# Optimization experiments

Measured on AMD Instinct MI355X. Metric: run time of the kernel, lower is better.

Reference implementation:

```python
import jax, jax.numpy as jnp
import numpy as np

GENE_DIM = 3000
DRUG_DIM = 2048
K = 6          # num_neurons_per_GO
KF = 24        # num_neurons_per_final_GO
T0, T1 = 1500, 400
OUT0, OUT1, OUT2 = T0 * K, T1 * K, KF
B = 256
NF = 64        # num_neurons_final
ND = [128, 64, 32]
EPS = 1e-5


def _edges():
    rng = np.random.default_rng(0)
    # level 0: each of T0 terms gets 30 genes, expanded to K neurons per term
    t = np.repeat(np.arange(T0), 30)
    g = rng.integers(0, GENE_DIM, T0 * 30)
    rows0 = (t[:, None] * K + np.arange(K)).ravel()
    cols0 = np.repeat(g, K)
    # level 1: each of T1 terms has 5 children among T0 terms, kron with ones(K,K)
    o = np.repeat(np.arange(T1), 5)
    c = rng.integers(0, T0, T1 * 5)
    P = len(o)
    rows1 = np.repeat(o, K * K) * K + np.tile(np.repeat(np.arange(K), K), P)
    cols1 = np.repeat(c, K * K) * K + np.tile(np.tile(np.arange(K), K), P)
    # level 2: single root with all T1 children, KF output neurons x K input neurons
    rows2 = np.tile(np.repeat(np.arange(KF), K), T1)
    cols2 = np.repeat(np.arange(T1), KF * K) * K + np.tile(np.arange(K), T1 * KF)
    return [(jnp.asarray(r, jnp.int32), jnp.asarray(cc, jnp.int32))
            for r, cc in ((rows0, cols0), (rows1, cols1), (rows2, cols2))]


def setup_inputs() -> dict:
    key = jax.random.key(0)
    ks = iter(jax.random.split(key, 64))
    (rows0, cols0), (rows1, cols1), (rows2, cols2) = _edges()
    nrm = lambda shape, s=0.1: s * jax.random.normal(next(ks), shape, jnp.float32)
    inp = {
        'x': jax.random.normal(next(ks), (B, GENE_DIM + DRUG_DIM), jnp.float32),
        'rows0': rows0, 'cols0': cols0, 'w0': nrm((rows0.shape[0],)), 'b0': nrm((OUT0,), 0.01),
        'rows1': rows1, 'cols1': cols1, 'w1': nrm((rows1.shape[0],)), 'b1': nrm((OUT1,), 0.01),
        'rows2': rows2, 'cols2': cols2, 'w2': nrm((rows2.shape[0],)), 'b2': nrm((OUT2,), 0.01),
        'gg': 1.0 + nrm((GENE_DIM,)), 'eg': nrm((GENE_DIM,), 0.01),
        'g1': 1.0 + nrm((OUT0,)), 'e1': nrm((OUT0,), 0.01),
        'g2': 1.0 + nrm((OUT1,)), 'e2': nrm((OUT1,), 0.01),
    }
    fan = DRUG_DIM
    for i, n in enumerate(ND, 1):
        inp[f'Wd{i}'] = nrm((n, fan), 1.0 / np.sqrt(fan))
        inp[f'bd{i}'] = nrm((n,), 0.01)
        inp[f'gd{i}'] = 1.0 + nrm((fan,))
        inp[f'ed{i}'] = nrm((fan,), 0.01)
        fan = n
    fin = KF + ND[-1]
    inp.update({
        'gf': 1.0 + nrm((fin,)), 'ef': nrm((fin,), 0.01),
        'Wf': nrm((NF, fin), 1.0 / np.sqrt(fin)), 'bf': nrm((NF,), 0.01),
        'ga': 1.0 + nrm((NF,)), 'ea': nrm((NF,), 0.01),
        'Wa': nrm((1, NF), 1.0 / np.sqrt(NF)), 'ba': nrm((1,), 0.01),
        'Wo': nrm((1, 1), 1.0), 'bo': nrm((1,), 0.01),
    })
    return inp


def _bn(x, g, e):
    # BatchNorm1d, training-mode batch statistics (biased var), dropout p=0
    mu = jnp.mean(x, 0)
    var = jnp.var(x, 0)
    return g * (x - mu) * jax.lax.rsqrt(var + EPS) + e


def _splin(x, rows, cols, w, b, n_out):
    # SparseLinear: y[b, rows[e]] += w[e] * x[b, cols[e]]
    data = (x[:, cols] * w).T                       # [E, B]
    return jax.ops.segment_sum(data, rows, num_segments=n_out).T + b


def reference(x, rows0, cols0, w0, b0, rows1, cols1, w1, b1, rows2, cols2, w2, b2,
              gg, eg, g1, e1, g2, e2,
              Wd1, bd1, gd1, ed1, Wd2, bd2, gd2, ed2, Wd3, bd3, gd3, ed3,
              gf, ef, Wf, bf, ga, ea, Wa, ba, Wo, bo):
    gene = x[:, :GENE_DIM]
    drug = x[:, GENE_DIM:GENE_DIM + DRUG_DIM]
    h = _bn(gene, gg, eg)
    h = jnp.tanh(_splin(h, rows0, cols0, w0, b0, OUT0))
    h = _bn(h, g1, e1)
    h = jnp.tanh(_splin(h, rows1, cols1, w1, b1, OUT1))
    h = _bn(h, g2, e2)
    h = jnp.tanh(_splin(h, rows2, cols2, w2, b2, OUT2))
    d = drug
    for (W, bb, g, e) in ((Wd1, bd1, gd1, ed1), (Wd2, bd2, gd2, ed2), (Wd3, bd3, gd3, ed3)):
        d = jnp.tanh(_bn(d, g, e) @ W.T + bb)
    o = _bn(jnp.concatenate([h, d], 1), gf, ef)
    o = jnp.tanh(o @ Wf.T + bf)
    o = _bn(o, ga, ea)
    o = jnp.tanh(o @ Wa.T + ba)
    return o @ Wo.T + bo
```

## Files before the change

kernel.cpp:

```cpp
#include <hip/hip_runtime.h>
#include <math.h>

#define NB 256
#define XW 5048
#define GENE 3000
#define DRUGW 2048
#define EPSF 1e-5f

template<int NR>
__device__ __forceinline__ void bn_fold_write(float (&v)[NR], int b,
        const float* __restrict__ g, const float* __restrict__ e,
        float* __restrict__ out_t) {
    __shared__ float sred[NR][4][2];
    __shared__ float s_ac[2][NR];
    int lane = b & 63, wv = b >> 6;
    float s1[NR], s2[NR];
    #pragma unroll
    for (int k = 0; k < NR; k++) { s1[k] = v[k]; s2[k] = v[k] * v[k]; }
    #pragma unroll
    for (int off = 32; off >= 1; off >>= 1) {
        #pragma unroll
        for (int k = 0; k < NR; k++) {
            s1[k] += __shfl_xor(s1[k], off);
            s2[k] += __shfl_xor(s2[k], off);
        }
    }
    if (lane == 0) {
        #pragma unroll
        for (int k = 0; k < NR; k++) { sred[k][wv][0] = s1[k]; sred[k][wv][1] = s2[k]; }
    }
    __syncthreads();
    if (b < NR) {
        float t1 = sred[b][0][0] + sred[b][1][0] + sred[b][2][0] + sred[b][3][0];
        float t2 = sred[b][0][1] + sred[b][1][1] + sred[b][2][1] + sred[b][3][1];
        float mu  = t1 * (1.0f / 256.0f);
        float var = t2 * (1.0f / 256.0f) - mu * mu;
        float rs  = rsqrtf(var + EPSF);
        float aa  = g[b] * rs;
        s_ac[0][b] = aa;
        s_ac[1][b] = e[b] - aa * mu;
    }
    __syncthreads();
    #pragma unroll
    for (int k = 0; k < NR; k++)
        out_t[k * NB + b] = s_ac[0][k] * v[k] + s_ac[1][k];
}

__global__ void k_in_bn(const float* __restrict__ x,
                        const float* __restrict__ gg, const float* __restrict__ eg,
                        const float* __restrict__ gd, const float* __restrict__ ed,
                        float* __restrict__ gene_n, float* __restrict__ drug_n) {
    __shared__ float tile[32 * 257];
    __shared__ float red1[8][33], red2[8][33];
    __shared__ float s_a[32], s_c[32];
    int t = threadIdx.x;
    int tx = t & 31, ty = t >> 5;
    int c0 = blockIdx.x * 32;
    int c = c0 + tx;
    bool valid = c < XW;
    float s1 = 0.f, s2 = 0.f;
    #pragma unroll 4
    for (int i = 0; i < 32; i++) {
        int r = ty * 32 + i;
        float v = valid ? x[(size_t)r * XW + c] : 0.f;
        tile[tx * 257 + r] = v;
        s1 += v; s2 += v * v;
    }
    red1[ty][tx] = s1; red2[ty][tx] = s2;
    __syncthreads();
    if (t < 32) {
        float t1 = 0.f, t2 = 0.f;
        #pragma unroll
        for (int k = 0; k < 8; k++) { t1 += red1[k][t]; t2 += red2[k][t]; }
        float mu  = t1 * (1.0f / 256.0f);
        float var = t2 * (1.0f / 256.0f) - mu * mu;
        float rs  = rsqrtf(var + EPSF);
        int col = c0 + t;
        float gv = 0.f, ev = 0.f;
        if (col < GENE)      { gv = gg[col];        ev = eg[col]; }
        else if (col < XW)   { gv = gd[col - GENE]; ev = ed[col - GENE]; }
        float aa = gv * rs;
        s_a[t] = aa; s_c[t] = ev - aa * mu;
    }
    __syncthreads();
    for (int cc = 0; cc < 32; cc++) {
        int col = c0 + cc;
        if (col >= XW) break;
        float w = s_a[cc] * tile[cc * 257 + t] + s_c[cc];
        if (col < GENE) gene_n[(size_t)col * NB + t] = w;
        else            drug_n[(size_t)(col - GENE) * NB + t] = w;
    }
}

__global__ void k_splin0(const float* __restrict__ gene_n,
                         const int* __restrict__ cols0, const float* __restrict__ w0,
                         const float* __restrict__ b0,
                         const float* __restrict__ g1, const float* __restrict__ e1,
                         float* __restrict__ h1n) {
    int t = blockIdx.x, b = threadIdx.x;
    float acc[6] = {0.f, 0.f, 0.f, 0.f, 0.f, 0.f};
    int base = t * 180;
    for (int i = 0; i < 30; i++) {
        int ei = base + i * 6;
        int cc = cols0[ei];
        float v = gene_n[(size_t)cc * NB + b];
        #pragma unroll
        for (int k = 0; k < 6; k++) acc[k] += v * w0[ei + k];
    }
    float v6[6];
    #pragma unroll
    for (int k = 0; k < 6; k++) v6[k] = tanhf(acc[k] + b0[t * 6 + k]);
    bn_fold_write<6>(v6, b, g1 + t * 6, e1 + t * 6, h1n + (size_t)t * 6 * NB);
}

__global__ void k_splin1(const float* __restrict__ h1n,
                         const int* __restrict__ cols1, const float* __restrict__ w1,
                         const float* __restrict__ b1,
                         const float* __restrict__ g2, const float* __restrict__ e2,
                         float* __restrict__ h2n) {
    int o = blockIdx.x, b = threadIdx.x;
    float acc[6] = {0.f, 0.f, 0.f, 0.f, 0.f, 0.f};
    for (int pi = 0; pi < 5; pi++) {
        int qb = (o * 5 + pi) * 36;
        #pragma unroll
        for (int j = 0; j < 6; j++) {
            int cc = cols1[qb + j];
            float v = h1n[(size_t)cc * NB + b];
            #pragma unroll
            for (int i = 0; i < 6; i++) acc[i] += v * w1[qb + i * 6 + j];
        }
    }
    float v6[6];
    #pragma unroll
    for (int i = 0; i < 6; i++) v6[i] = tanhf(acc[i] + b1[o * 6 + i]);
    bn_fold_write<6>(v6, b, g2 + o * 6, e2 + o * 6, h2n + (size_t)o * 6 * NB);
}

__global__ void k_splin2_part(const float* __restrict__ h2n,
                              const float* __restrict__ w2,
                              float* __restrict__ part2) {
    int kf = blockIdx.x >> 4, ch = blockIdx.x & 15, b = threadIdx.x;
    float acc = 0.f;
    int t0 = ch * 25;
    for (int t = t0; t < t0 + 25; t++) {
        const float* wrow = w2 + t * 144 + kf * 6;
        #pragma unroll
        for (int j = 0; j < 6; j++)
            acc += h2n[(size_t)(t * 6 + j) * NB + b] * wrow[j];
    }
    part2[(size_t)blockIdx.x * NB + b] = acc;
}

__global__ void k_splin2_fin(const float* __restrict__ part2,
                             const float* __restrict__ b2,
                             const float* __restrict__ gf, const float* __restrict__ ef,
                             float* __restrict__ fbn) {
    int kf = blockIdx.x, b = threadIdx.x;
    float acc = b2[kf];
    #pragma unroll
    for (int ch = 0; ch < 16; ch++) acc += part2[(size_t)(kf * 16 + ch) * NB + b];
    float v[1] = { tanhf(acc) };
    bn_fold_write<1>(v, b, gf + kf, ef + kf, fbn + (size_t)kf * NB);
}

__global__ void k_dense1_part(const float* __restrict__ drug_n,
                              const float* __restrict__ Wd1,
                              float* __restrict__ part1) {
    int jg = blockIdx.x >> 3, ch = blockIdx.x & 7, b = threadIdx.x;
    int j0 = jg * 4, c0 = ch * 256;
    float acc[4] = {0.f, 0.f, 0.f, 0.f};
    for (int c = c0; c < c0 + 256; c++) {
        float v = drug_n[(size_t)c * NB + b];
        #pragma unroll
        for (int jj = 0; jj < 4; jj++) acc[jj] += v * Wd1[(size_t)(j0 + jj) * DRUGW + c];
    }
    #pragma unroll
    for (int jj = 0; jj < 4; jj++)
        part1[(size_t)((j0 + jj) * 8 + ch) * NB + b] = acc[jj];
}

__global__ void k_dense1_fin(const float* __restrict__ part1,
                             const float* __restrict__ bd1,
                             const float* __restrict__ gd2, const float* __restrict__ ed2,
                             float* __restrict__ d1n) {
    int j = blockIdx.x, b = threadIdx.x;
    float acc = bd1[j];
    #pragma unroll
    for (int ch = 0; ch < 8; ch++) acc += part1[(size_t)(j * 8 + ch) * NB + b];
    float v[1] = { tanhf(acc) };
    bn_fold_write<1>(v, b, gd2 + j, ed2 + j, d1n + (size_t)j * NB);
}

template<int JPB>
__global__ void k_dense_n(const float* __restrict__ in_n,
                          const float* __restrict__ W, const float* __restrict__ bias,
                          int ncols,
                          const float* __restrict__ g, const float* __restrict__ e,
                          float* __restrict__ out_n) {
    int j0 = blockIdx.x * JPB, b = threadIdx.x;
    float acc[JPB];
    #pragma unroll
    for (int jj = 0; jj < JPB; jj++) acc[jj] = 0.f;
    for (int c = 0; c < ncols; c++) {
        float v = in_n[(size_t)c * NB + b];
        #pragma unroll
        for (int jj = 0; jj < JPB; jj++) acc[jj] += v * W[(size_t)(j0 + jj) * ncols + c];
    }
    float v[JPB];
    #pragma unroll
    for (int jj = 0; jj < JPB; jj++) v[jj] = tanhf(acc[jj] + bias[j0 + jj]);
    bn_fold_write<JPB>(v, b, g + j0, e + j0, out_n + (size_t)j0 * NB);
}

__global__ void k_final(const float* __restrict__ o1n,
                        const float* __restrict__ Wa, const float* __restrict__ ba,
                        const float* __restrict__ Wo, const float* __restrict__ bo,
                        float* __restrict__ out) {
    int b = threadIdx.x;
    float acc = ba[0];
    #pragma unroll
    for (int j = 0; j < 64; j++) acc += o1n[(size_t)j * NB + b] * Wa[j];
    out[b] = tanhf(acc) * Wo[0] + bo[0];
}

extern "C" void kernel_launch(void* const* d_in, const int* in_sizes, int n_in,
                              void* d_out, int out_size, void* d_ws, size_t ws_size,
                              hipStream_t stream) {
    const float* x    = (const float*)d_in[0];
    const int*   cols0 = (const int*)d_in[2];
    const float* w0   = (const float*)d_in[3];
    const float* b0   = (const float*)d_in[4];
    const int*   cols1 = (const int*)d_in[6];
    const float* w1   = (const float*)d_in[7];
    const float* b1   = (const float*)d_in[8];
    const float* w2   = (const float*)d_in[11];
    const float* b2   = (const float*)d_in[12];
    const float* gg   = (const float*)d_in[13];
    const float* eg   = (const float*)d_in[14];
    const float* g1   = (const float*)d_in[15];
    const float* e1   = (const float*)d_in[16];
    const float* g2   = (const float*)d_in[17];
    const float* e2   = (const float*)d_in[18];
    const float* Wd1  = (const float*)d_in[19];
    const float* bd1  = (const float*)d_in[20];
    const float* gd1  = (const float*)d_in[21];
    const float* ed1  = (const float*)d_in[22];
    const float* Wd2  = (const float*)d_in[23];
    const float* bd2  = (const float*)d_in[24];
    const float* gd2  = (const float*)d_in[25];
    const float* ed2  = (const float*)d_in[26];
    const float* Wd3  = (const float*)d_in[27];
    const float* bd3  = (const float*)d_in[28];
    const float* gd3  = (const float*)d_in[29];
    const float* ed3  = (const float*)d_in[30];
    const float* gf   = (const float*)d_in[31];
    const float* ef   = (const float*)d_in[32];
    const float* Wf   = (const float*)d_in[33];
    const float* bf   = (const float*)d_in[34];
    const float* ga   = (const float*)d_in[35];
    const float* ea   = (const float*)d_in[36];
    const float* Wa   = (const float*)d_in[37];
    const float* ba   = (const float*)d_in[38];
    const float* Wo   = (const float*)d_in[39];
    const float* bo   = (const float*)d_in[40];
    float* out = (float*)d_out;

    float* W = (float*)d_ws;
    float* gene_n = W;
    float* drug_n = gene_n + 3000 * NB;
    float* h1n    = drug_n + 2048 * NB;
    float* h2n    = h1n    + 9000 * NB;
    float* fbn    = h2n    + 2400 * NB;
    float* d1n    = fbn    + 56 * NB;
    float* d2n    = d1n    + 128 * NB;
    float* o1n    = d2n    + 64 * NB;
    float* part2  = o1n    + 64 * NB;
    float* part1  = part2  + 24 * 16 * NB;

    k_in_bn<<<(XW + 31) / 32, 256, 0, stream>>>(x, gg, eg, gd1, ed1, gene_n, drug_n);

    k_splin0<<<1500, 256, 0, stream>>>(gene_n, cols0, w0, b0, g1, e1, h1n);
    k_splin1<<<400, 256, 0, stream>>>(h1n, cols1, w1, b1, g2, e2, h2n);
    k_splin2_part<<<24 * 16, 256, 0, stream>>>(h2n, w2, part2);
    k_splin2_fin<<<24, 256, 0, stream>>>(part2, b2, gf, ef, fbn);

    k_dense1_part<<<32 * 8, 256, 0, stream>>>(drug_n, Wd1, part1);
    k_dense1_fin<<<128, 256, 0, stream>>>(part1, bd1, gd2, ed2, d1n);
    k_dense_n<8><<<8, 256, 0, stream>>>(d1n, Wd2, bd2, 128, gd3, ed3, d2n);
    k_dense_n<8><<<4, 256, 0, stream>>>(d2n, Wd3, bd3, 64, gf + 24, ef + 24, fbn + 24 * NB);

    k_dense_n<8><<<8, 256, 0, stream>>>(fbn, Wf, bf, 56, ga, ea, o1n);
    k_final<<<1, 256, 0, stream>>>(o1n, Wa, ba, Wo, bo, out);
}
```

Baseline: 148.9 us.

## Fuse all stages into one persistent kernel with atomic grid barriers

Replaces the eleven separate kernel launches with a single persistent kernel of 256 blocks. Stages are separated by a software grid barrier built on an atomic counter, and independent work such as the gene and drug branches is packed into the same phase. Intermediate activations h1 and h2 are stored batch-interleaved so later stages can use float2 loads, and splin2 now computes all 24 outputs per chunk. This removes launch gaps and per-kernel tails, at the cost of spin-wait barriers, lower parallelism in the small stages, and a memset launch to reset the counter.

```diff
diff --git a/kernel.cpp b/kernel.cpp
--- a/kernel.cpp
+++ b/kernel.cpp
@@ -6,11 +6,49 @@
 #define GENE 3000
 #define DRUGW 2048
 #define EPSF 1e-5f
-
-template<int NR>
-__device__ __forceinline__ void bn_fold_write(float (&v)[NR], int b,
+#define NBLK 256
+
+struct Params {
+    const float* x;
+    const int* cols0; const float* w0; const float* b0;
+    const int* cols1; const float* w1; const float* b1;
+    const float* w2;  const float* b2;
+    const float* gg;  const float* eg;
+    const float* g1;  const float* e1;
+    const float* g2;  const float* e2;
+    const float* Wd1; const float* bd1;
+    const float* gd1; const float* ed1;
+    const float* Wd2; const float* bd2;
+    const float* gd2; const float* ed2;
+    const float* Wd3; const float* bd3;
+    const float* gd3; const float* ed3;
+    const float* gf;  const float* ef;
+    const float* Wf;  const float* bf;
+    const float* ga;  const float* ea;
+    const float* Wa;  const float* ba;
+    const float* Wo;  const float* bo;
+    float* out;
+    float* gene_n; float* drug_n; float* h1i; float* h2i;
+    float* fbn; float* d1n; float* d2n; float* o1n; float* part2; float* part1;
+    unsigned int* bar;
+};
+
+__device__ __forceinline__ void gbar(unsigned int* bar, unsigned int target) {
+    __syncthreads();
+    if (threadIdx.x == 0) {
+        __threadfence();
+        __hip_atomic_fetch_add(bar, 1u, __ATOMIC_RELEASE, __HIP_MEMORY_SCOPE_AGENT);
+        while (__hip_atomic_load(bar, __ATOMIC_ACQUIRE, __HIP_MEMORY_SCOPE_AGENT) < target)
+            __builtin_amdgcn_s_sleep(2);
+        __threadfence();
+    }
+    __syncthreads();
+}
+
+template<int NR, bool ILEAVE>
+__device__ __forceinline__ void bn_fold(float (&v)[NR], int b,
         const float* __restrict__ g, const float* __restrict__ e,
-        float* __restrict__ out_t) {
+        float* __restrict__ out) {
     __shared__ float sred[NR][4][2];
     __shared__ float s_ac[2][NR];
     int lane = b & 63, wv = b >> 6;
@@ -42,43 +80,40 @@
     }
     __syncthreads();
     #pragma unroll
-    for (int k = 0; k < NR; k++)
-        out_t[k * NB + b] = s_ac[0][k] * v[k] + s_ac[1][k];
-}
-
-__global__ void k_in_bn(const float* __restrict__ x,
-                        const float* __restrict__ gg, const float* __restrict__ eg,
-                        const float* __restrict__ gd, const float* __restrict__ ed,
-                        float* __restrict__ gene_n, float* __restrict__ drug_n) {
-    __shared__ float tile[32 * 257];
-    __shared__ float red1[8][33], red2[8][33];
-    __shared__ float s_a[32], s_c[32];
-    int t = threadIdx.x;
+    for (int k = 0; k < NR; k++) {
+        float w = s_ac[0][k] * v[k] + s_ac[1][k];
+        if (ILEAVE) out[b * NR + k] = w;
+        else        out[k * NB + b] = w;
+    }
+}
+
+__device__ __forceinline__ void inbn_task(const Params& p, int task, int t,
+        float* tile, float* red1, float* red2, float* s_a, float* s_c) {
     int tx = t & 31, ty = t >> 5;
-    int c0 = blockIdx.x * 32;
+    int c0 = task * 32;
     int c = c0 + tx;
     bool valid = c < XW;
     float s1 = 0.f, s2 = 0.f;
     #pragma unroll 4
     for (int i = 0; i < 32; i++) {
         int r = ty * 32 + i;
-        float v = valid ? x[(size_t)r * XW + c] : 0.f;
+        float v = valid ? p.x[(size_t)r * XW + c] : 0.f;
         tile[tx * 257 + r] = v;
         s1 += v; s2 += v * v;
     }
-    red1[ty][tx] = s1; red2[ty][tx] = s2;
+    red1[ty * 33 + tx] = s1; red2[ty * 33 + tx] = s2;
     __syncthreads();
     if (t < 32) {
         float t1 = 0.f, t2 = 0.f;
         #pragma unroll
-        for (int k = 0; k < 8; k++) { t1 += red1[k][t]; t2 += red2[k][t]; }
+        for (int k = 0; k < 8; k++) { t1 += red1[k * 33 + t]; t2 += red2[k * 33 + t]; }
         float mu  = t1 * (1.0f / 256.0f);
         float var = t2 * (1.0f / 256.0f) - mu * mu;
         float rs  = rsqrtf(var + EPSF);
         int col = c0 + t;
         float gv = 0.f, ev = 0.f;
-        if (col < GENE)      { gv = gg[col];        ev = eg[col]; }
-        else if (col < XW)   { gv = gd[col - GENE]; ev = ed[col - GENE]; }
+        if (col < GENE)      { gv = p.gg[col];         ev = p.eg[col]; }
+        else if (col < XW)   { gv = p.gd1[col - GENE]; ev = p.ed1[col - GENE]; }
         float aa = gv * rs;
         s_a[t] = aa; s_c[t] = ev - aa * mu;
     }
@@ -87,208 +122,223 @@
         int col = c0 + cc;
         if (col >= XW) break;
         float w = s_a[cc] * tile[cc * 257 + t] + s_c[cc];
-        if (col < GENE) gene_n[(size_t)col * NB + t] = w;
-        else            drug_n[(size_t)(col - GENE) * NB + t] = w;
-    }
-}
-
-__global__ void k_splin0(const float* __restrict__ gene_n,
-                         const int* __restrict__ cols0, const float* __restrict__ w0,
-                         const float* __restrict__ b0,
-                         const float* __restrict__ g1, const float* __restrict__ e1,
-                         float* __restrict__ h1n) {
-    int t = blockIdx.x, b = threadIdx.x;
+        if (col < GENE) p.gene_n[(size_t)col * NB + t] = w;
+        else            p.drug_n[(size_t)(col - GENE) * NB + t] = w;
+    }
+    __syncthreads();
+}
+
+__device__ __forceinline__ void splin0_task(const Params& p, int t, int b) {
     float acc[6] = {0.f, 0.f, 0.f, 0.f, 0.f, 0.f};
     int base = t * 180;
     for (int i = 0; i < 30; i++) {
         int ei = base + i * 6;
-        int cc = cols0[ei];
-        float v = gene_n[(size_t)cc * NB + b];
-        #pragma unroll
-        for (int k = 0; k < 6; k++) acc[k] += v * w0[ei + k];
+        int cc = p.cols0[ei];
+        float v = p.gene_n[(size_t)cc * NB + b];
+        #pragma unroll
+        for (int k = 0; k < 6; k++) acc[k] += v * p.w0[ei + k];
     }
     float v6[6];
     #pragma unroll
-    for (int k = 0; k < 6; k++) v6[k] = tanhf(acc[k] + b0[t * 6 + k]);
-    bn_fold_write<6>(v6, b, g1 + t * 6, e1 + t * 6, h1n + (size_t)t * 6 * NB);
-}
-
-__global__ void k_splin1(const float* __restrict__ h1n,
-                         const int* __restrict__ cols1, const float* __restrict__ w1,
-                         const float* __restrict__ b1,
-                         const float* __restrict__ g2, const float* __restrict__ e2,
-                         float* __restrict__ h2n) {
-    int o = blockIdx.x, b = threadIdx.x;
+    for (int k = 0; k < 6; k++) v6[k] = tanhf(acc[k] + p.b0[t * 6 + k]);
+    bn_fold<6, true>(v6, b, p.g1 + t * 6, p.e1 + t * 6, p.h1i + (size_t)t * 6 * NB);
+}
+
+__device__ __forceinline__ void splin1_task(const Params& p, int o, int b) {
     float acc[6] = {0.f, 0.f, 0.f, 0.f, 0.f, 0.f};
     for (int pi = 0; pi < 5; pi++) {
         int qb = (o * 5 + pi) * 36;
-        #pragma unroll
-        for (int j = 0; j < 6; j++) {
-            int cc = cols1[qb + j];
-            float v = h1n[(size_t)cc * NB + b];
+        int cbase = p.cols1[qb];
+        const float* hv = p.h1i + (size_t)cbase * NB + b * 6;
+        const float2* hv2 = (const float2*)hv;
+        float2 a0 = hv2[0], a1 = hv2[1], a2 = hv2[2];
+        float v[6] = {a0.x, a0.y, a1.x, a1.y, a2.x, a2.y};
+        #pragma unroll
+        for (int j = 0; j < 6; j++)
             #pragma unroll
-            for (int i = 0; i < 6; i++) acc[i] += v * w1[qb + i * 6 + j];
-        }
+            for (int i = 0; i < 6; i++) acc[i] += v[j] * p.w1[qb + i * 6 + j];
     }
     float v6[6];
     #pragma unroll
-    for (int i = 0; i < 6; i++) v6[i] = tanhf(acc[i] + b1[o * 6 + i]);
-    bn_fold_write<6>(v6, b, g2 + o * 6, e2 + o * 6, h2n + (size_t)o * 6 * NB);
-}
-
-__global__ void k_splin2_part(const float* __restrict__ h2n,
-                              const float* __restrict__ w2,
-                              float* __restrict__ part2) {
-    int kf = blockIdx.x >> 4, ch = blockIdx.x & 15, b = threadIdx.x;
-    float acc = 0.f;
+    for (int i = 0; i < 6; i++) v6[i] = tanhf(acc[i] + p.b1[o * 6 + i]);
+    bn_fold<6, true>(v6, b, p.g2 + o * 6, p.e2 + o * 6, p.h2i + (size_t)o * 6 * NB);
+}
+
+__device__ __forceinline__ void splin2_part_task(const Params& p, int ch, int b) {
+    float acc[24];
+    #pragma unroll
+    for (int kf = 0; kf < 24; kf++) acc[kf] = 0.f;
     int t0 = ch * 25;
     for (int t = t0; t < t0 + 25; t++) {
-        const float* wrow = w2 + t * 144 + kf * 6;
-        #pragma unroll
-        for (int j = 0; j < 6; j++)
-            acc += h2n[(size_t)(t * 6 + j) * NB + b] * wrow[j];
-    }
-    part2[(size_t)blockIdx.x * NB + b] = acc;
-}
-
-__global__ void k_splin2_fin(const float* __restrict__ part2,
-                             const float* __restrict__ b2,
-                             const float* __restrict__ gf, const float* __restrict__ ef,
-                             float* __restrict__ fbn) {
-    int kf = blockIdx.x, b = threadIdx.x;
-    float acc = b2[kf];
-    #pragma unroll
-    for (int ch = 0; ch < 16; ch++) acc += part2[(size_t)(kf * 16 + ch) * NB + b];
+        const float* hv = p.h2i + (size_t)t * 6 * NB + b * 6;
+        const float2* hv2 = (const float2*)hv;
+        float2 a0 = hv2[0], a1 = hv2[1], a2 = hv2[2];
+        float v[6] = {a0.x, a0.y, a1.x, a1.y, a2.x, a2.y};
+        const float* wr = p.w2 + t * 144;
+        #pragma unroll
+        for (int kf = 0; kf < 24; kf++)
+            #pragma unroll
+            for (int j = 0; j < 6; j++) acc[kf] += v[j] * wr[kf * 6 + j];
+    }
+    #pragma unroll
+    for (int kf = 0; kf < 24; kf++)
+        p.part2[(size_t)(ch * 24 + kf) * NB + b] = acc[kf];
+}
+
+__device__ __forceinline__ void splin2_fin_task(const Params& p, int kf, int b) {
+    float acc = p.b2[kf];
+    #pragma unroll
+    for (int ch = 0; ch < 16; ch++) acc += p.part2[(size_t)(ch * 24 + kf) * NB + b];
     float v[1] = { tanhf(acc) };
-    bn_fold_write<1>(v, b, gf + kf, ef + kf, fbn + (size_t)kf * NB);
-}
-
-__global__ void k_dense1_part(const float* __restrict__ drug_n,
-                              const float* __restrict__ Wd1,
-                              float* __restrict__ part1) {
-    int jg = blockIdx.x >> 3, ch = blockIdx.x & 7, b = threadIdx.x;
+    bn_fold<1, false>(v, b, p.gf + kf, p.ef + kf, p.fbn + (size_t)kf * NB);
+}
+
+__device__ __forceinline__ void dense1_part_task(const Params& p, int sub, int b) {
+    int jg = sub >> 3, ch = sub & 7;
     int j0 = jg * 4, c0 = ch * 256;
     float acc[4] = {0.f, 0.f, 0.f, 0.f};
     for (int c = c0; c < c0 + 256; c++) {
-        float v = drug_n[(size_t)c * NB + b];
-        #pragma unroll
-        for (int jj = 0; jj < 4; jj++) acc[jj] += v * Wd1[(size_t)(j0 + jj) * DRUGW + c];
+        float v = p.drug_n[(size_t)c * NB + b];
+        #pragma unroll
+        for (int jj = 0; jj < 4; jj++) acc[jj] += v * p.Wd1[(size_t)(j0 + jj) * DRUGW + c];
     }
     #pragma unroll
     for (int jj = 0; jj < 4; jj++)
-        part1[(size_t)((j0 + jj) * 8 + ch) * NB + b] = acc[jj];
-}
-
-__global__ void k_dense1_fin(const float* __restrict__ part1,
-                             const float* __restrict__ bd1,
-                             const float* __restrict__ gd2, const float* __restrict__ ed2,
-                             float* __restrict__ d1n) {
-    int j = blockIdx.x, b = threadIdx.x;
-    float acc = bd1[j];
-    #pragma unroll
-    for (int ch = 0; ch < 8; ch++) acc += part1[(size_t)(j * 8 + ch) * NB + b];
+        p.part1[(size_t)((j0 + jj) * 8 + ch) * NB + b] = acc[jj];
+}
+
+__device__ __forceinline__ void dense1_fin_task(const Params& p, int j, int b) {
+    float acc = p.bd1[j];
+    #pragma unroll
+    for (int ch = 0; ch < 8; ch++) acc += p.part1[(size_t)(j * 8 + ch) * NB + b];
     float v[1] = { tanhf(acc) };
-    bn_fold_write<1>(v, b, gd2 + j, ed2 + j, d1n + (size_t)j * NB);
-}
-
-template<int JPB>
-__global__ void k_dense_n(const float* __restrict__ in_n,
-                          const float* __restrict__ W, const float* __restrict__ bias,
-                          int ncols,
-                          const float* __restrict__ g, const float* __restrict__ e,
-                          float* __restrict__ out_n) {
-    int j0 = blockIdx.x * JPB, b = threadIdx.x;
-    float acc[JPB];
-    #pragma unroll
-    for (int jj = 0; jj < JPB; jj++) acc[jj] = 0.f;
+    bn_fold<1, false>(v, b, p.gd2 + j, p.ed2 + j, p.d1n + (size_t)j * NB);
+}
+
+__device__ __forceinline__ void dense8_task(const float* __restrict__ in_n,
+        const float* __restrict__ W, const float* __restrict__ bias, int ncols,
+        const float* __restrict__ g, const float* __restrict__ e,
+        float* __restrict__ out_n, int j0, int b) {
+    float acc[8] = {0.f,0.f,0.f,0.f,0.f,0.f,0.f,0.f};
     for (int c = 0; c < ncols; c++) {
         float v = in_n[(size_t)c * NB + b];
         #pragma unroll
-        for (int jj = 0; jj < JPB; jj++) acc[jj] += v * W[(size_t)(j0 + jj) * ncols + c];
-    }
-    float v[JPB];
-    #pragma unroll
-    for (int jj = 0; jj < JPB; jj++) v[jj] = tanhf(acc[jj] + bias[j0 + jj]);
-    bn_fold_write<JPB>(v, b, g + j0, e + j0, out_n + (size_t)j0 * NB);
-}
-
-__global__ void k_final(const float* __restrict__ o1n,
-                        const float* __restrict__ Wa, const float* __restrict__ ba,
-                        const float* __restrict__ Wo, const float* __restrict__ bo,
-                        float* __restrict__ out) {
-    int b = threadIdx.x;
-    float acc = ba[0];
-    #pragma unroll
-    for (int j = 0; j < 64; j++) acc += o1n[(size_t)j * NB + b] * Wa[j];
-    out[b] = tanhf(acc) * Wo[0] + bo[0];
+        for (int jj = 0; jj < 8; jj++) acc[jj] += v * W[(size_t)(j0 + jj) * ncols + c];
+    }
+    float v[8];
+    #pragma unroll
+    for (int jj = 0; jj < 8; jj++) v[jj] = tanhf(acc[jj] + bias[j0 + jj]);
+    bn_fold<8, false>(v, b, g + j0, e + j0, out_n + (size_t)j0 * NB);
+}
+
+__device__ __forceinline__ void final_task(const Params& p, int b) {
+    float acc = p.ba[0];
+    #pragma unroll
+    for (int j = 0; j < 64; j++) acc += p.o1n[(size_t)j * NB + b] * p.Wa[j];
+    p.out[b] = tanhf(acc) * p.Wo[0] + p.bo[0];
+}
+
+__global__ __launch_bounds__(256) void k_mega(Params p) {
+    __shared__ float tile[32 * 257];
+    __shared__ float red1[8 * 33];
+    __shared__ float red2[8 * 33];
+    __shared__ float s_a[32], s_c[32];
+    const int b = threadIdx.x;
+
+    for (int task = blockIdx.x; task < 158; task += gridDim.x)
+        inbn_task(p, task, b, tile, red1, red2, s_a, s_c);
+    gbar(p.bar, 1 * NBLK);
+
+    for (int task = blockIdx.x; task < 1756; task += gridDim.x) {
+        if (task < 1500) splin0_task(p, task, b);
+        else             dense1_part_task(p, task - 1500, b);
+    }
+    gbar(p.bar, 2 * NBLK);
+
+    for (int task = blockIdx.x; task < 528; task += gridDim.x) {
+        if (task < 400) splin1_task(p, task, b);
+        else            dense1_fin_task(p, task - 400, b);
+    }
+    gbar(p.bar, 3 * NBLK);
+
+    for (int task = blockIdx.x; task < 24; task += gridDim.x) {
+        if (task < 16) splin2_part_task(p, task, b);
+        else dense8_task(p.d1n, p.Wd2, p.bd2, 128, p.gd3, p.ed3, p.d2n, (task - 16) * 8, b);
+    }
+    gbar(p.bar, 4 * NBLK);
+
+    for (int task = blockIdx.x; task < 28; task += gridDim.x) {
+        if (task < 24) splin2_fin_task(p, task, b);
+        else dense8_task(p.d2n, p.Wd3, p.bd3, 64, p.gf + 24, p.ef + 24,
+                         p.fbn + 24 * NB, (task - 24) * 8, b);
+    }
+    gbar(p.bar, 5 * NBLK);
+
+    for (int task = blockIdx.x; task < 8; task += gridDim.x)
+        dense8_task(p.fbn, p.Wf, p.bf, 56, p.ga, p.ea, p.o1n, task * 8, b);
+    gbar(p.bar, 6 * NBLK);
+
+    if (blockIdx.x == 0)
+        final_task(p, b);
 }
 
 extern "C" void kernel_launch(void* const* d_in, const int* in_sizes, int n_in,
                               void* d_out, int out_size, void* d_ws, size_t ws_size,
                               hipStream_t stream) {
-    const float* x    = (const float*)d_in[0];
-    const int*   cols0 = (const int*)d_in[2];
-    const float* w0   = (const float*)d_in[3];
-    const float* b0   = (const float*)d_in[4];
-    const int*   cols1 = (const int*)d_in[6];
-    const float* w1   = (const float*)d_in[7];
-    const float* b1   = (const float*)d_in[8];
-    const float* w2   = (const float*)d_in[11];
-    const float* b2   = (const float*)d_in[12];
-    const float* gg   = (const float*)d_in[13];
-    const float* eg   = (const float*)d_in[14];
-    const float* g1   = (const float*)d_in[15];
-    const float* e1   = (const float*)d_in[16];
-    const float* g2   = (const float*)d_in[17];
-    const float* e2   = (const float*)d_in[18];
-    const float* Wd1  = (const float*)d_in[19];
-    const float* bd1  = (const float*)d_in[20];
-    const float* gd1  = (const float*)d_in[21];
-    const float* ed1  = (const float*)d_in[22];
-    const float* Wd2  = (const float*)d_in[23];
-    const float* bd2  = (const float*)d_in[24];
-    const float* gd2  = (const float*)d_in[25];
-    const float* ed2  = (const float*)d_in[26];
-    const float* Wd3  = (const float*)d_in[27];
-    const float* bd3  = (const float*)d_in[28];
-    const float* gd3  = (const float*)d_in[29];
-    const float* ed3  = (const float*)d_in[30];
-    const float* gf   = (const float*)d_in[31];
-    const float* ef   = (const float*)d_in[32];
-    const float* Wf   = (const float*)d_in[33];
-    const float* bf   = (const float*)d_in[34];
-    const float* ga   = (const float*)d_in[35];
-    const float* ea   = (const float*)d_in[36];
-    const float* Wa   = (const float*)d_in[37];
-    const float* ba   = (const float*)d_in[38];
-    const float* Wo   = (const float*)d_in[39];
-    const float* bo   = (const float*)d_in[40];
-    float* out = (float*)d_out;
+    Params p;
+    p.x    = (const float*)d_in[0];
+    p.cols0 = (const int*)d_in[2];
+    p.w0   = (const float*)d_in[3];
+    p.b0   = (const float*)d_in[4];
+    p.cols1 = (const int*)d_in[6];
+    p.w1   = (const float*)d_in[7];
+    p.b1   = (const float*)d_in[8];
+    p.w2   = (const float*)d_in[11];
+    p.b2   = (const float*)d_in[12];
+    p.gg   = (const float*)d_in[13];
+    p.eg   = (const float*)d_in[14];
+    p.g1   = (const float*)d_in[15];
+    p.e1   = (const float*)d_in[16];
+    p.g2   = (const float*)d_in[17];
+    p.e2   = (const float*)d_in[18];
+    p.Wd1  = (const float*)d_in[19];
+    p.bd1  = (const float*)d_in[20];
+    p.gd1  = (const float*)d_in[21];
+    p.ed1  = (const float*)d_in[22];
+    p.Wd2  = (const float*)d_in[23];
+    p.bd2  = (const float*)d_in[24];
+    p.gd2  = (const float*)d_in[25];
+    p.ed2  = (const float*)d_in[26];
+    p.Wd3  = (const float*)d_in[27];
+    p.bd3  = (const float*)d_in[28];
+    p.gd3  = (const float*)d_in[29];
+    p.ed3  = (const float*)d_in[30];
+    p.gf   = (const float*)d_in[31];
+    p.ef   = (const float*)d_in[32];
+    p.Wf   = (const float*)d_in[33];
+    p.bf   = (const float*)d_in[34];
+    p.ga   = (const float*)d_in[35];
+    p.ea   = (const float*)d_in[36];
+    p.Wa   = (const float*)d_in[37];
+    p.ba   = (const float*)d_in[38];
+    p.Wo   = (const float*)d_in[39];
+    p.bo   = (const float*)d_in[40];
+    p.out  = (float*)d_out;
 
     float* W = (float*)d_ws;
-    float* gene_n = W;
-    float* drug_n = gene_n + 3000 * NB;
-    float* h1n    = drug_n + 2048 * NB;
-    float* h2n    = h1n    + 9000 * NB;
-    float* fbn    = h2n    + 2400 * NB;
-    float* d1n    = fbn    + 56 * NB;
-    float* d2n    = d1n    + 128 * NB;
-    float* o1n    = d2n    + 64 * NB;
-    float* part2  = o1n    + 64 * NB;
-    float* part1  = part2  + 24 * 16 * NB;
-
-    k_in_bn<<<(XW + 31) / 32, 256, 0, stream>>>(x, gg, eg, gd1, ed1, gene_n, drug_n);
-
-    k_splin0<<<1500, 256, 0, stream>>>(gene_n, cols0, w0, b0, g1, e1, h1n);
-    k_splin1<<<400, 256, 0, stream>>>(h1n, cols1, w1, b1, g2, e2, h2n);
-    k_splin2_part<<<24 * 16, 256, 0, stream>>>(h2n, w2, part2);
-    k_splin2_fin<<<24, 256, 0, stream>>>(part2, b2, gf, ef, fbn);
-
-    k_dense1_part<<<32 * 8, 256, 0, stream>>>(drug_n, Wd1, part1);
-    k_dense1_fin<<<128, 256, 0, stream>>>(part1, bd1, gd2, ed2, d1n);
-    k_dense_n<8><<<8, 256, 0, stream>>>(d1n, Wd2, bd2, 128, gd3, ed3, d2n);
-    k_dense_n<8><<<4, 256, 0, stream>>>(d2n, Wd3, bd3, 64, gf + 24, ef + 24, fbn + 24 * NB);
-
-    k_dense_n<8><<<8, 256, 0, stream>>>(fbn, Wf, bf, 56, ga, ea, o1n);
-    k_final<<<1, 256, 0, stream>>>(o1n, Wa, ba, Wo, bo, out);
-}
+    p.gene_n = W;
+    p.drug_n = p.gene_n + 3000 * NB;
+    p.h1i    = p.drug_n + 2048 * NB;
+    p.h2i    = p.h1i    + 9000 * NB;
+    p.fbn    = p.h2i    + 2400 * NB;
+    p.d1n    = p.fbn    + 56 * NB;
+    p.d2n    = p.d1n    + 128 * NB;
+    p.o1n    = p.d2n    + 64 * NB;
+    p.part2  = p.o1n    + 64 * NB;
+    p.part1  = p.part2  + 16 * 24 * NB;
+    p.bar    = (unsigned int*)(p.part1 + 128 * 8 * NB);
+
+    hipMemsetAsync((void*)p.bar, 0, 64, stream);
+
+    k_mega<<<dim3(NBLK), dim3(256), 0, stream>>>(p);
+}
```

Result: slower. 359.8 us (+141.6%).
